# Optimization experiments

Measured on AMD Instinct MI355X. Metric: run time of the kernel, lower is better.

Reference implementation:

```python
import jax, jax.numpy as jnp
import numpy as np

N = 4096    # nodes per graph
C = 128     # in_channels == out_channels
HEAD = 1
E = 65536   # edges per graph (avg degree 16)


def setup_inputs() -> dict:
    key = jax.random.key(0)
    ks = jax.random.split(key, 24)
    def w(k, shape):
        return jax.random.normal(k, shape, dtype=jnp.float32) * 0.05
    return {
        "x1": jax.random.normal(ks[0], (N, C), dtype=jnp.float32),
        "x2": jax.random.normal(ks[1], (N, C), dtype=jnp.float32),
        "edge_index1": jax.random.randint(ks[2], (2, E), 0, N),
        "edge_index2": jax.random.randint(ks[3], (2, E), 0, N),
        "wl1_w": w(ks[4], (HEAD * C, C)), "wl1_b": w(ks[5], (HEAD * C,)),
        "wr1_w": w(ks[6], (HEAD * C, C)), "wr1_b": w(ks[7], (HEAD * C,)),
        "al1": w(ks[8], (HEAD, C)), "ar1": w(ks[9], (HEAD, C)),
        "wl2_w": w(ks[10], (HEAD * C, C)), "wl2_b": w(ks[11], (HEAD * C,)),
        "wr2_w": w(ks[12], (HEAD * C, C)), "wr2_b": w(ks[13], (HEAD * C,)),
        "al2": w(ks[14], (HEAD, C)), "ar2": w(ks[15], (HEAD, C)),
        "w1_w": w(ks[16], (C, 2 * C)), "w1_b": w(ks[17], (C,)),
        "w2_w": w(ks[18], (C, 2 * C)), "w2_b": w(ks[19], (C,)),
        "lin_w": w(ks[20], (HEAD * C, C)), "lin_b": w(ks[21], (HEAD * C,)),
    }


def _leaky_relu(x):
    return jnp.where(x > 0, x, 0.2 * x)


def _attention(src, tgt, wl, bl, wr, br, al, ar):
    # alpha_l: (N_src,), alpha_r: (N_tot,) -> dense (N_src, N_tot) softmax
    a_l = ((src @ wl.T + bl).reshape(-1, HEAD, C) * al[None]).sum(-1).mean(1)
    a_r = ((tgt @ wr.T + br).reshape(-1, HEAD, C) * ar[None]).sum(-1).mean(1)
    return jax.nn.softmax(_leaky_relu(a_l[:, None] + a_r[None, :]), axis=1)


def _aggr_update(x_i, tgt_all, ei, wl, bl, wr, br, al, ar, ww, wb):
    att = _attention(x_i, tgt_all, wl, bl, wr, br, al, ar)   # (N_i, N_tot)
    ot = x_i - att @ tgt_all                                  # (N_i, C)
    feat = jnp.concatenate([x_i, ot], axis=1)                 # (N_i, 2C)
    n = x_i.shape[0]
    loops = jnp.arange(n)                                     # add_self_loops
    src = jnp.concatenate([ei[0], loops])
    dst = jnp.concatenate([ei[1], loops])
    sums = jax.ops.segment_sum(feat[dst], src, num_segments=n)
    cnt = jax.ops.segment_sum(jnp.ones((src.shape[0],), feat.dtype), src, num_segments=n)
    aggr = sums / cnt[:, None]                                # scatter 'mean'
    return jax.nn.relu(aggr) @ ww.T + wb


def reference(x1, x2, edge_index1, edge_index2,
              wl1_w, wl1_b, wr1_w, wr1_b, al1, ar1,
              wl2_w, wl2_b, wr2_w, wr2_b, al2, ar2,
              w1_w, w1_b, w2_w, w2_b, lin_w, lin_b):
    Xs = [x1, x2]
    eis = [edge_index1, edge_index2]
    layers = [(wl1_w, wl1_b, wr1_w, wr1_b, al1, ar1, w1_w, w1_b),
              (wl2_w, wl2_b, wr2_w, wr2_b, al2, ar2, w2_w, w2_b)]
    for (wl, bl, wr, br, al, ar, ww, wb) in layers:
        tgt = jnp.concatenate(Xs, axis=0)
        Xs = [_aggr_update(Xs[i], tgt, eis[i], wl, bl, wr, br, al, ar, ww, wb)
              for i in range(2)]
    feats = jnp.concatenate(Xs, axis=0) @ lin_w.T + lin_b     # (2N, C)
    return jax.nn.sigmoid(feats @ feats.T)                    # (2N, 2N)
```

## Files before the change

### kernel.cpp

```cpp
#include <hip/hip_runtime.h>
#include <hip/hip_bf16.h>

#define NT 8192
#define NN 4096
#define CD 128
#define NE 65536

typedef __attribute__((ext_vector_type(8))) short bf16x8;
typedef __attribute__((ext_vector_type(16))) float f32x16;
typedef __attribute__((ext_vector_type(4))) float f32x4;

__global__ __launch_bounds__(256) void k_prep(
    const float* __restrict__ W1, const float* __restrict__ W2, const float* __restrict__ WL,
    float* __restrict__ WT1, float* __restrict__ WT2, float* __restrict__ WTL,
    const float* __restrict__ wlw0, const float* __restrict__ wlb0,
    const float* __restrict__ wrw0, const float* __restrict__ wrb0,
    const float* __restrict__ al0, const float* __restrict__ ar0,
    const float* __restrict__ wlw1, const float* __restrict__ wlb1,
    const float* __restrict__ wrw1, const float* __restrict__ wrb1,
    const float* __restrict__ al1, const float* __restrict__ ar1,
    float* __restrict__ VP, int* __restrict__ DEG) {
  int b = blockIdx.x, tid = threadIdx.x;
  if (b < 320) {
    int idx = b * 256 + tid;
    if (idx < 32768) { int c = idx >> 8, k = idx & 255; WT1[k * 128 + c] = W1[idx]; }
    else if (idx < 65536) { int j = idx - 32768; int c = j >> 8, k = j & 255; WT2[k * 128 + c] = W2[j]; }
    else { int j = idx - 65536; int c = j >> 7, k = j & 127; WTL[k * 128 + c] = WL[j]; }
  } else if (b < 322) {
    int L = b - 320;
    const float* wlw = L ? wlw1 : wlw0;
    const float* wlb = L ? wlb1 : wlb0;
    const float* wrw = L ? wrw1 : wrw0;
    const float* wrb = L ? wrb1 : wrb0;
    const float* alv = L ? al1 : al0;
    const float* arv = L ? ar1 : ar0;
    float* vp = VP + L * 258;
    if (tid < 128) {
      int c = tid;
      float sl = 0.f, sr = 0.f;
      for (int h = 0; h < 128; ++h) {
        sl += wlw[h * 128 + c] * alv[h];
        sr += wrw[h * 128 + c] * arv[h];
      }
      vp[c] = sl;
      vp[128 + c] = sr;
      if (c < 2) {
        const float* bb = c ? wrb : wlb;
        const float* aa = c ? arv : alv;
        float s = 0.f;
        for (int h = 0; h < 128; ++h) s += bb[h] * aa[h];
        vp[256 + c] = s;
      }
    }
  } else {
    int idx = (b - 322) * 256 + tid;
    DEG[idx] = 0;
  }
}

__global__ void k_deg(const int* __restrict__ EI1, const int* __restrict__ EI2,
                      int* __restrict__ DEG) {
  int idx = blockIdx.x * 256 + threadIdx.x;
  int g = idx >> 16, e = idx & 65535;
  const int* src = g ? EI2 : EI1;
  atomicAdd(&DEG[g * NN + src[e]], 1);
}

__global__ void k_scanoff(const int* __restrict__ DEG, int* __restrict__ OFFS,
                          int* __restrict__ CURS) {
  int g = blockIdx.x, tid = threadIdx.x;
  __shared__ int part[256];
  int loc[16];
  int s = 0;
  #pragma unroll
  for (int i = 0; i < 16; ++i) { loc[i] = s; s += DEG[g * NN + tid * 16 + i]; }
  part[tid] = s;
  __syncthreads();
  for (int d = 1; d < 256; d <<= 1) {
    int v = part[tid];
    int o = (tid >= d) ? part[tid - d] : 0;
    __syncthreads();
    part[tid] = v + o;
    __syncthreads();
  }
  int excl = tid ? part[tid - 1] : 0;
  #pragma unroll
  for (int i = 0; i < 16; ++i) {
    int o = excl + loc[i];
    OFFS[g * (NN + 1) + tid * 16 + i] = o;
    CURS[g * NN + tid * 16 + i] = o;
  }
  if (tid == 255) OFFS[g * (NN + 1) + NN] = part[255];
}

__global__ void k_fill(const int* __restrict__ EI1, const int* __restrict__ EI2,
                       int* __restrict__ CURS, int* __restrict__ ADJ) {
  int idx = blockIdx.x * 256 + threadIdx.x;
  int g = idx >> 16, e = idx & 65535;
  const int* ei = g ? EI2 : EI1;
  int s = ei[e], d = ei[NE + e];
  int pos = atomicAdd(&CURS[g * NN + s], 1);
  ADJ[g * NE + pos] = d;
}

__global__ void k_alar(const float* __restrict__ X, const float* __restrict__ VP,
                       float* __restrict__ AL, float* __restrict__ AR,
                       int* __restrict__ RANK) {
  if (blockIdx.x < 32) RANK[blockIdx.x * 256 + threadIdx.x] = 0;
  int lane = threadIdx.x & 63;
  int row = blockIdx.x * 4 + (threadIdx.x >> 6);
  float x0 = X[row * 128 + lane], x1 = X[row * 128 + 64 + lane];
  float sl = x0 * VP[lane] + x1 * VP[64 + lane];
  float sr = x0 * VP[128 + lane] + x1 * VP[192 + lane];
  #pragma unroll
  for (int m = 1; m < 64; m <<= 1) {
    sl += __shfl_xor(sl, m, 64);
    sr += __shfl_xor(sr, m, 64);
  }
  if (lane == 0) { AL[row] = sl + VP[256]; AR[row] = sr + VP[257]; }
}

__global__ void k_rank(const float* __restrict__ AR, int* __restrict__ RANK) {
  __shared__ float tile[1024];
  int j = blockIdx.x * 256 + threadIdx.x;
  int base = blockIdx.y * 1024;
  for (int t = threadIdx.x; t < 1024; t += 256) tile[t] = AR[base + t];
  __syncthreads();
  float aj = AR[j];
  int cnt = 0;
  #pragma unroll 8
  for (int u = 0; u < 1024; ++u) {
    float a2 = tile[u];
    cnt += (a2 < aj || (a2 == aj && (base + u) < j)) ? 1 : 0;
  }
  atomicAdd(&RANK[j], cnt);
}

__global__ void k_perm(const int* __restrict__ RANK, const float* __restrict__ AR,
                       int* __restrict__ PERM, float* __restrict__ ARS) {
  int j = blockIdx.x * 256 + threadIdx.x;
  int r = RANK[j];
  PERM[r] = j;
  ARS[r] = AR[j];
}

__global__ __launch_bounds__(320) void k_scanA(
    const float* __restrict__ X, const int* __restrict__ PERM,
    const float* __restrict__ ARS,
    float* __restrict__ P1, float* __restrict__ P2,
    float* __restrict__ CT1, float* __restrict__ CT2,
    float* __restrict__ Q1L, float* __restrict__ Q2L,
    float* __restrict__ QCT1, float* __restrict__ QCT2) {
  __shared__ int pc[64];
  __shared__ float w1[64], w2[64];
  int chunk = blockIdx.x, tid = threadIdx.x;
  if (tid < 64) {
    int r = chunk * 64 + tid;
    pc[tid] = PERM[r];
    float a = ARS[r];
    w1[tid] = __expf(a);
    w2[tid] = __expf(0.2f * a);
  }
  __syncthreads();
  if (tid < 128) {
    int c = tid;
    float acc = 0.f;
    #pragma unroll 4
    for (int t = 0; t < 64; ++t) {
      acc += w1[t] * X[pc[t] * 128 + c];
      P1[(chunk * 64 + t) * 128 + c] = acc;
    }
    CT1[chunk * 128 + c] = acc;
  } else if (tid < 256) {
    int c = tid - 128;
    float acc = 0.f;
    #pragma unroll 4
    for (int t = 0; t < 64; ++t) {
      acc += w2[t] * X[pc[t] * 128 + c];
      P2[(chunk * 64 + t) * 128 + c] = acc;
    }
    CT2[chunk * 128 + c] = acc;
  } else if (tid == 256) {
    float acc = 0.f;
    for (int t = 0; t < 64; ++t) { acc += w1[t]; Q1L[chunk * 64 + t] = acc; }
    QCT1[chunk] = acc;
  } else if (tid == 257) {
    float acc = 0.f;
    for (int t = 0; t < 64; ++t) { acc += w2[t]; Q2L[chunk * 64 + t] = acc; }
    QCT2[chunk] = acc;
  }
}

__global__ __launch_bounds__(320) void k_scanB(
    const float* __restrict__ CT1, const float* __restrict__ CT2,
    const float* __restrict__ QCT1, const float* __restrict__ QCT2,
    float* __restrict__ OFF1, float* __restrict__ OFF2,
    float* __restrict__ QOF1, float* __restrict__ QOF2) {
  int tid = threadIdx.x;
  if (tid < 128) {
    float acc = 0.f;
    #pragma unroll 8
    for (int ch = 0; ch < 128; ++ch) { acc += CT1[ch * 128 + tid]; OFF1[ch * 128 + tid] = acc; }
  } else if (tid < 256) {
    int c = tid - 128;
    float acc = 0.f;
    #pragma unroll 8
    for (int ch = 0; ch < 128; ++ch) { acc += CT2[ch * 128 + c]; OFF2[ch * 128 + c] = acc; }
  } else if (tid == 256) {
    float acc = 0.f;
    for (int ch = 0; ch < 128; ++ch) { acc += QCT1[ch]; QOF1[ch] = acc; }
  } else if (tid == 257) {
    float acc = 0.f;
    for (int ch = 0; ch < 128; ++ch) { acc += QCT2[ch]; QOF2[ch] = acc; }
  }
}

__global__ void k_combine(const float* __restrict__ X, const float* __restrict__ AL,
                          const float* __restrict__ ARS,
                          const float* __restrict__ P1, const float* __restrict__ P2,
                          const float* __restrict__ OFF1, const float* __restrict__ OFF2,
                          const float* __restrict__ Q1L, const float* __restrict__ Q2L,
                          const float* __restrict__ QOF1, const float* __restrict__ QOF2,
                          float* __restrict__ OT) {
  int row = blockIdx.x * 2 + (threadIdx.x >> 7);
  int c = threadIdx.x & 127;
  float ali = AL[row];
  float A1 = __expf(ali), A2 = __expf(0.2f * ali);
  float xv = -ali;
  int lo = 0, hi = NT;
  while (lo < hi) {
    int mid = (lo + hi) >> 1;
    if (ARS[mid] <= xv) lo = mid + 1; else hi = mid;
  }
  int b = lo - 1;
  float p1 = 0.f, p2 = 0.f, q1 = 0.f, q2 = 0.f;
  if (b >= 0) {
    int ch = b >> 6;
    p1 = P1[b * 128 + c] + (ch ? OFF1[(ch - 1) * 128 + c] : 0.f);
    p2 = P2[b * 128 + c] + (ch ? OFF2[(ch - 1) * 128 + c] : 0.f);
    q1 = Q1L[b] + (ch ? QOF1[ch - 1] : 0.f);
    q2 = Q2L[b] + (ch ? QOF2[ch - 1] : 0.f);
  }
  float T1 = OFF1[127 * 128 + c];
  float QT1 = QOF1[127];
  float num = A1 * (T1 - p1) + A2 * p2;
  float den = A1 * (QT1 - q1) + A2 * q2;
  OT[row * 128 + c] = X[row * 128 + c] - num / den;
}

__global__ __launch_bounds__(256) void k_aggr(const float* __restrict__ X,
                                              const float* __restrict__ OT,
                                              const int* __restrict__ OFFS,
                                              const int* __restrict__ ADJ,
                                              float* __restrict__ AGGR) {
  int node = blockIdx.x * 4 + (threadIdx.x >> 6);
  int lane = threadIdx.x & 63;
  int g = node >> 12, n = node & (NN - 1);
  const int* off = OFFS + g * (NN + 1);
  const int* adj = ADJ + g * NE;
  int beg = off[n], end = off[n + 1];
  const f32x4* src = (const f32x4*)((lane < 32 ? X : OT) + (size_t)g * NN * CD);
  int c4 = lane & 31;
  f32x4 acc = src[n * 32 + c4];
  for (int e = beg; e < end; ++e) {
    int d = adj[e];
    acc += src[d * 32 + c4];
  }
  f32x4 r = acc / (float)(end - beg + 1);
  ((f32x4*)AGGR)[(size_t)node * 64 + (lane < 32 ? c4 : 32 + c4)] = r;
}

template <int KD, bool RELU, bool OBF>
__global__ __launch_bounds__(128) void k_gemm(const float* __restrict__ A,
                                              const float* __restrict__ WT,
                                              const float* __restrict__ bias,
                                              void* __restrict__ out) {
  __shared__ float sA[8 * KD];
  int c = threadIdx.x;
  int r0 = blockIdx.x * 8;
  for (int i = c; i < 8 * KD; i += 128) {
    float a = A[(size_t)r0 * KD + i];
    if (RELU) a = fmaxf(a, 0.f);
    sA[i] = a;
  }
  __syncthreads();
  float acc[8];
  float bc = bias[c];
  #pragma unroll
  for (int i = 0; i < 8; ++i) acc[i] = bc;
  for (int k = 0; k < KD; ++k) {
    float wv = WT[k * 128 + c];
    #pragma unroll
    for (int i = 0; i < 8; ++i) acc[i] += sA[i * KD + k] * wv;
  }
  if (OBF) {
    __hip_bfloat16* o = (__hip_bfloat16*)out;
    #pragma unroll
    for (int i = 0; i < 8; ++i) o[(r0 + i) * 128 + c] = __float2bfloat16(acc[i]);
  } else {
    float* o = (float*)out;
    #pragma unroll
    for (int i = 0; i < 8; ++i) o[(r0 + i) * 128 + c] = acc[i];
  }
}

__device__ inline f32x16 zero16() {
  f32x16 v;
  #pragma unroll
  for (int i = 0; i < 16; ++i) v[i] = 0.f;
  return v;
}

__device__ inline void store_frag(float* __restrict__ out, const f32x16& a,
                                  int grow0, int gcol) {
  #pragma unroll
  for (int r = 0; r < 16; ++r) {
    int rloc = (r & 3) + 8 * (r >> 2);
    float v = a[r];
    out[(size_t)(grow0 + rloc) * 8192 + gcol] =
        __builtin_amdgcn_rcpf(1.f + __expf(-v));
  }
}

__global__ __launch_bounds__(256) void k_final(const unsigned short* __restrict__ F,
                                               float* __restrict__ out) {
  __shared__ unsigned short AT[128 * 128];
  __shared__ unsigned short BT[128 * 128];
  int cb = blockIdx.x, rb = blockIdx.y;
  int tid = threadIdx.x;
  #pragma unroll
  for (int q = 0; q < 8; ++q) {
    int idx = q * 256 + tid;
    int r = idx >> 4, ck = idx & 15;
    unsigned off = (unsigned)((r * 256 + ck * 16) ^ ((r & 7) << 4));
    uint4 va = *(const uint4*)(F + (size_t)(rb * 128 + r) * 128 + ck * 8);
    *(uint4*)((char*)AT + off) = va;
    uint4 vb = *(const uint4*)(F + (size_t)(cb * 128 + r) * 128 + ck * 8);
    *(uint4*)((char*)BT + off) = vb;
  }
  __syncthreads();
  int lane = tid & 63, w = tid >> 6;
  int wr = w >> 1, wc = w & 1;
  int l31 = lane & 31, kh = lane >> 5;
  int xorm = (l31 & 7) << 4;
  int rowA0 = wr * 64 + l31, rowA1 = rowA0 + 32;
  int rowB0 = wc * 64 + l31, rowB1 = rowB0 + 32;
  f32x16 a00 = zero16(), a01 = zero16(), a10 = zero16(), a11 = zero16();
  #pragma unroll
  for (int ks = 0; ks < 8; ++ks) {
    int kb = ks * 32 + kh * 16;
    bf16x8 av0 = *(const bf16x8*)((const char*)AT + ((rowA0 * 256 + kb) ^ xorm));
    bf16x8 av1 = *(const bf16x8*)((const char*)AT + ((rowA1 * 256 + kb) ^ xorm));
    bf16x8 bv0 = *(const bf16x8*)((const char*)BT + ((rowB0 * 256 + kb) ^ xorm));
    bf16x8 bv1 = *(const bf16x8*)((const char*)BT + ((rowB1 * 256 + kb) ^ xorm));
    a00 = __builtin_amdgcn_mfma_f32_32x32x16_bf16(av0, bv0, a00, 0, 0, 0);
    a01 = __builtin_amdgcn_mfma_f32_32x32x16_bf16(av0, bv1, a01, 0, 0, 0);
    a10 = __builtin_amdgcn_mfma_f32_32x32x16_bf16(av1, bv0, a10, 0, 0, 0);
    a11 = __builtin_amdgcn_mfma_f32_32x32x16_bf16(av1, bv1, a11, 0, 0, 0);
  }
  int grow = rb * 128 + wr * 64 + 4 * kh;
  int gcol = cb * 128 + wc * 64 + l31;
  store_frag(out, a00, grow, gcol);
  store_frag(out, a01, grow, gcol + 32);
  store_frag(out, a10, grow + 32, gcol);
  store_frag(out, a11, grow + 32, gcol + 32);
}

extern "C" void kernel_launch(void* const* d_in, const int* in_sizes, int n_in,
                              void* d_out, int out_size, void* d_ws, size_t ws_size,
                              hipStream_t stream) {
  (void)in_sizes; (void)n_in; (void)out_size; (void)ws_size;
  const float* x1 = (const float*)d_in[0];
  const float* x2 = (const float*)d_in[1];
  const int* ei1 = (const int*)d_in[2];
  const int* ei2 = (const int*)d_in[3];
  const float* wl_w[2] = {(const float*)d_in[4], (const float*)d_in[10]};
  const float* wl_b[2] = {(const float*)d_in[5], (const float*)d_in[11]};
  const float* wr_w[2] = {(const float*)d_in[6], (const float*)d_in[12]};
  const float* wr_b[2] = {(const float*)d_in[7], (const float*)d_in[13]};
  const float* alv[2] = {(const float*)d_in[8], (const float*)d_in[14]};
  const float* arv[2] = {(const float*)d_in[9], (const float*)d_in[15]};
  const float* ww_w[2] = {(const float*)d_in[16], (const float*)d_in[18]};
  const float* ww_b[2] = {(const float*)d_in[17], (const float*)d_in[19]};
  const float* lin_w = (const float*)d_in[20];
  const float* lin_b = (const float*)d_in[21];

  char* wp = (char*)d_ws;
  auto alloc = [&](size_t b) -> char* {
    char* p = wp;
    wp += (b + 255) & ~(size_t)255;
    return p;
  };
  float* XA = (float*)alloc((size_t)NT * CD * 4);
  float* XB = (float*)alloc((size_t)NT * CD * 4);
  float* OT = (float*)alloc((size_t)NT * CD * 4);
  float* P1 = (float*)alloc((size_t)NT * CD * 4);
  float* P2 = (float*)alloc((size_t)NT * CD * 4);
  float* AGGR = P1;
  float* CT1 = (float*)alloc(128 * 128 * 4);
  float* CT2 = (float*)alloc(128 * 128 * 4);
  float* OFF1 = (float*)alloc(128 * 128 * 4);
  float* OFF2 = (float*)alloc(128 * 128 * 4);
  float* AL = (float*)alloc(NT * 4);
  float* AR_ = (float*)alloc(NT * 4);
  float* ARS = (float*)alloc(NT * 4);
  float* Q1L = (float*)alloc(NT * 4);
  float* Q2L = (float*)alloc(NT * 4);
  float* QCT1 = (float*)alloc(128 * 4);
  float* QCT2 = (float*)alloc(128 * 4);
  float* QOF1 = (float*)alloc(128 * 4);
  float* QOF2 = (float*)alloc(128 * 4);
  float* VP = (float*)alloc(2 * 258 * 4);
  float* WT1 = (float*)alloc(256 * 128 * 4);
  float* WT2 = (float*)alloc(256 * 128 * 4);
  float* WTL = (float*)alloc(128 * 128 * 4);
  int* RANK = (int*)alloc(NT * 4);
  int* PERM = (int*)alloc(NT * 4);
  int* DEG = (int*)alloc(2 * NN * 4);
  int* OFFS = (int*)alloc(2 * (NN + 1) * 4);
  int* CURS = (int*)alloc(2 * NN * 4);
  int* ADJ = (int*)alloc(2 * NE * 4);
  unsigned short* FBF = (unsigned short*)OT;

  hipMemcpyAsync(XA, x1, (size_t)NN * CD * 4, hipMemcpyDeviceToDevice, stream);
  hipMemcpyAsync(XA + (size_t)NN * CD, x2, (size_t)NN * CD * 4, hipMemcpyDeviceToDevice, stream);
  k_prep<<<354, 256, 0, stream>>>(ww_w[0], ww_w[1], lin_w, WT1, WT2, WTL,
                                  wl_w[0], wl_b[0], wr_w[0], wr_b[0], alv[0], arv[0],
                                  wl_w[1], wl_b[1], wr_w[1], wr_b[1], alv[1], arv[1],
                                  VP, DEG);
  k_deg<<<512, 256, 0, stream>>>(ei1, ei2, DEG);
  k_scanoff<<<2, 256, 0, stream>>>(DEG, OFFS, CURS);
  k_fill<<<512, 256, 0, stream>>>(ei1, ei2, CURS, ADJ);

  float* X = XA;
  float* XN = XB;
  for (int L = 0; L < 2; ++L) {
    k_alar<<<2048, 256, 0, stream>>>(X, VP + L * 258, AL, AR_, RANK);
    k_rank<<<dim3(32, 8), 256, 0, stream>>>(AR_, RANK);
    k_perm<<<32, 256, 0, stream>>>(RANK, AR_, PERM, ARS);
    k_scanA<<<128, 320, 0, stream>>>(X, PERM, ARS, P1, P2, CT1, CT2, Q1L, Q2L, QCT1, QCT2);
    k_scanB<<<1, 320, 0, stream>>>(CT1, CT2, QCT1, QCT2, OFF1, OFF2, QOF1, QOF2);
    k_combine<<<4096, 256, 0, stream>>>(X, AL, ARS, P1, P2, OFF1, OFF2, Q1L, Q2L, QOF1, QOF2, OT);
    k_aggr<<<2048, 256, 0, stream>>>(X, OT, OFFS, ADJ, AGGR);
    k_gemm<256, true, false><<<1024, 128, 0, stream>>>(AGGR, L ? WT2 : WT1, ww_b[L], XN);
    float* t = X; X = XN; XN = t;
  }
  k_gemm<128, false, true><<<1024, 128, 0, stream>>>(X, WTL, lin_b, FBF);
  k_final<<<dim3(64, 64), 256, 0, stream>>>(FBF, (float*)d_out);
}
```

Baseline: 322.4 us.

## Fuse pipeline stages into fewer launches with last-block tail reductions

```diff
diff --git a/kernel.cpp b/kernel.cpp
--- a/kernel.cpp
+++ b/kernel.cpp
@@ -5,12 +5,24 @@
 #define NN 4096
 #define CD 128
 #define NE 65536
+#define SCOPE_AGT __HIP_MEMORY_SCOPE_AGENT
 
 typedef __attribute__((ext_vector_type(8))) short bf16x8;
 typedef __attribute__((ext_vector_type(16))) float f32x16;
 typedef __attribute__((ext_vector_type(4))) float f32x4;
 
+__device__ inline void stg_f(float* p, float v) {
+  __hip_atomic_store(p, v, __ATOMIC_RELAXED, SCOPE_AGT);
+}
+__device__ inline float ldg_f(const float* p) {
+  return __hip_atomic_load(p, __ATOMIC_RELAXED, SCOPE_AGT);
+}
+__device__ inline int ldg_i(const int* p) {
+  return __hip_atomic_load(p, __ATOMIC_RELAXED, SCOPE_AGT);
+}
+
 __global__ __launch_bounds__(256) void k_prep(
+    const float* __restrict__ x1, const float* __restrict__ x2, float* __restrict__ X,
     const float* __restrict__ W1, const float* __restrict__ W2, const float* __restrict__ WL,
     float* __restrict__ WT1, float* __restrict__ WT2, float* __restrict__ WTL,
     const float* __restrict__ wlw0, const float* __restrict__ wlb0,
@@ -19,15 +31,24 @@
     const float* __restrict__ wlw1, const float* __restrict__ wlb1,
     const float* __restrict__ wrw1, const float* __restrict__ wrb1,
     const float* __restrict__ al1, const float* __restrict__ ar1,
-    float* __restrict__ VP, int* __restrict__ DEG) {
+    float* __restrict__ VP, int* __restrict__ DEG, int* __restrict__ TK) {
   int b = blockIdx.x, tid = threadIdx.x;
-  if (b < 320) {
-    int idx = b * 256 + tid;
+  int gid = b * 256 + tid;
+  {
+    const f32x4* s1 = (const f32x4*)x1;
+    const f32x4* s2 = (const f32x4*)x2;
+    f32x4* d = (f32x4*)X;
+    d[gid] = s1[gid];
+    d[gid + NN * CD / 4] = s2[gid];
+  }
+  if (gid < 81920) {
+    int idx = gid;
     if (idx < 32768) { int c = idx >> 8, k = idx & 255; WT1[k * 128 + c] = W1[idx]; }
     else if (idx < 65536) { int j = idx - 32768; int c = j >> 8, k = j & 255; WT2[k * 128 + c] = W2[j]; }
     else { int j = idx - 65536; int c = j >> 7, k = j & 127; WTL[k * 128 + c] = WL[j]; }
-  } else if (b < 322) {
-    int L = b - 320;
+  }
+  if ((b == 508 || b == 509) && tid < 128) {
+    int L = b - 508;
     const float* wlw = L ? wlw1 : wlw0;
     const float* wlb = L ? wlb1 : wlb0;
     const float* wrw = L ? wrw1 : wrw0;
@@ -35,40 +56,159 @@
     const float* alv = L ? al1 : al0;
     const float* arv = L ? ar1 : ar0;
     float* vp = VP + L * 258;
-    if (tid < 128) {
-      int c = tid;
-      float sl = 0.f, sr = 0.f;
-      for (int h = 0; h < 128; ++h) {
-        sl += wlw[h * 128 + c] * alv[h];
-        sr += wrw[h * 128 + c] * arv[h];
-      }
-      vp[c] = sl;
-      vp[128 + c] = sr;
-      if (c < 2) {
-        const float* bb = c ? wrb : wlb;
-        const float* aa = c ? arv : alv;
-        float s = 0.f;
-        for (int h = 0; h < 128; ++h) s += bb[h] * aa[h];
-        vp[256 + c] = s;
-      }
-    }
+    int c = tid;
+    float sl = 0.f, sr = 0.f;
+    for (int h = 0; h < 128; ++h) {
+      sl += wlw[h * 128 + c] * alv[h];
+      sr += wrw[h * 128 + c] * arv[h];
+    }
+    vp[c] = sl;
+    vp[128 + c] = sr;
+    if (c < 2) {
+      const float* bb = c ? wrb : wlb;
+      const float* aa = c ? arv : alv;
+      float s = 0.f;
+      for (int h = 0; h < 128; ++h) s += bb[h] * aa[h];
+      vp[256 + c] = s;
+    }
+  }
+  if (gid < 2 * NN) DEG[gid] = 0;
+  if (b == 0 && tid < 8) TK[tid] = 0;
+}
+
+__device__ void alar_row(const float* __restrict__ X, const float* __restrict__ VP,
+                         float* __restrict__ AL, float* __restrict__ AR,
+                         int row, int lane) {
+  float x0 = X[row * 128 + lane], x1 = X[row * 128 + 64 + lane];
+  float sl = x0 * VP[lane] + x1 * VP[64 + lane];
+  float sr = x0 * VP[128 + lane] + x1 * VP[192 + lane];
+  #pragma unroll
+  for (int m = 1; m < 64; m <<= 1) {
+    sl += __shfl_xor(sl, m, 64);
+    sr += __shfl_xor(sr, m, 64);
+  }
+  if (lane == 0) { AL[row] = sl + VP[256]; AR[row] = sr + VP[257]; }
+}
+
+__device__ void rankperm_body(int rb, int tid, const float* __restrict__ AR,
+                              int* __restrict__ RANK, int* __restrict__ PERM,
+                              float* __restrict__ ARS, int* __restrict__ TK, int slot) {
+  __shared__ float tile[1024];
+  __shared__ int isLast;
+  int jb = rb & 31, tb = rb >> 5;
+  int base = tb * 1024;
+  for (int t = tid; t < 1024; t += 256) tile[t] = AR[base + t];
+  __syncthreads();
+  int j = jb * 256 + tid;
+  float aj = AR[j];
+  int cnt = 0;
+  #pragma unroll 8
+  for (int u = 0; u < 1024; ++u) {
+    float a2 = tile[u];
+    cnt += (a2 < aj || (a2 == aj && (base + u) < j)) ? 1 : 0;
+  }
+  atomicAdd(&RANK[j], cnt);
+  __threadfence();
+  __syncthreads();
+  if (tid == 0) {
+    int t = __hip_atomic_fetch_add(&TK[slot], 1, __ATOMIC_ACQ_REL, SCOPE_AGT);
+    isLast = (t == 255);
+  }
+  __syncthreads();
+  if (isLast) {
+    for (int jj = tid; jj < NT; jj += 256) {
+      int rk = ldg_i(&RANK[jj]);
+      PERM[rk] = jj;
+      ARS[rk] = AR[jj];
+    }
+  }
+}
+
+__device__ void scanA_body(int chunk, int tid, const float* __restrict__ X,
+                           const int* __restrict__ PERM, const float* __restrict__ ARS,
+                           float* __restrict__ P1, float* __restrict__ P2,
+                           float* __restrict__ CT1, float* __restrict__ CT2,
+                           float* __restrict__ Q1L, float* __restrict__ Q2L,
+                           float* __restrict__ QCT1, float* __restrict__ QCT2,
+                           float* __restrict__ OFF1, float* __restrict__ OFF2,
+                           float* __restrict__ QOF1, float* __restrict__ QOF2,
+                           int* __restrict__ TK, int slot) {
+  __shared__ float sm[192];
+  __shared__ int isLast;
+  int* pc = (int*)sm;
+  float* w1 = sm + 64;
+  float* w2 = sm + 128;
+  if (tid < 64) {
+    int r = chunk * 64 + tid;
+    pc[tid] = PERM[r];
+    float a = ARS[r];
+    w1[tid] = __expf(a);
+    w2[tid] = __expf(0.2f * a);
+  }
+  __syncthreads();
+  int c = tid & 127;
+  {
+    const float* W = (tid < 128) ? w1 : w2;
+    float* P = (tid < 128) ? P1 : P2;
+    float* CT = (tid < 128) ? CT1 : CT2;
+    float acc = 0.f;
+    #pragma unroll 4
+    for (int t = 0; t < 64; ++t) {
+      acc += W[t] * X[pc[t] * 128 + c];
+      P[(chunk * 64 + t) * 128 + c] = acc;
+    }
+    stg_f(&CT[chunk * 128 + c], acc);
+  }
+  if (tid < 2) {
+    const float* Wq = tid ? w2 : w1;
+    float* Q = tid ? Q2L : Q1L;
+    float* QC = tid ? QCT2 : QCT1;
+    float qa = 0.f;
+    for (int t = 0; t < 64; ++t) { qa += Wq[t]; Q[chunk * 64 + t] = qa; }
+    stg_f(&QC[chunk], qa);
+  }
+  __threadfence();
+  __syncthreads();
+  if (tid == 0) {
+    int t = __hip_atomic_fetch_add(&TK[slot], 1, __ATOMIC_ACQ_REL, SCOPE_AGT);
+    isLast = (t == 127);
+  }
+  __syncthreads();
+  if (isLast) {
+    const float* CTs = (tid < 128) ? CT1 : CT2;
+    float* OFF = (tid < 128) ? OFF1 : OFF2;
+    float a2 = 0.f;
+    #pragma unroll 8
+    for (int ch = 0; ch < 128; ++ch) { a2 += ldg_f(&CTs[ch * 128 + c]); OFF[ch * 128 + c] = a2; }
+    if (tid < 2) {
+      const float* QC = tid ? QCT2 : QCT1;
+      float* QO = tid ? QOF2 : QOF1;
+      float qa = 0.f;
+      for (int ch = 0; ch < 128; ++ch) { qa += ldg_f(&QC[ch]); QO[ch] = qa; }
+    }
+  }
+}
+
+__global__ __launch_bounds__(256) void k_stage2(
+    const int* __restrict__ EI1, const int* __restrict__ EI2, int* __restrict__ DEG,
+    const float* __restrict__ X, const float* __restrict__ VP0,
+    float* __restrict__ AL, float* __restrict__ AR, int* __restrict__ RANK) {
+  int b = blockIdx.x, tid = threadIdx.x;
+  if (b < 512) {
+    int gid = b * 256 + tid;
+    int g = gid >> 16, e = gid & 65535;
+    const int* src = g ? EI2 : EI1;
+    atomicAdd(&DEG[g * NN + src[e]], 1);
   } else {
-    int idx = (b - 322) * 256 + tid;
-    DEG[idx] = 0;
-  }
-}
-
-__global__ void k_deg(const int* __restrict__ EI1, const int* __restrict__ EI2,
-                      int* __restrict__ DEG) {
-  int idx = blockIdx.x * 256 + threadIdx.x;
-  int g = idx >> 16, e = idx & 65535;
-  const int* src = g ? EI2 : EI1;
-  atomicAdd(&DEG[g * NN + src[e]], 1);
-}
-
-__global__ void k_scanoff(const int* __restrict__ DEG, int* __restrict__ OFFS,
-                          int* __restrict__ CURS) {
-  int g = blockIdx.x, tid = threadIdx.x;
+    int bb = b - 512;
+    int gid = bb * 256 + tid;
+    if (gid < NT) RANK[gid] = 0;
+    alar_row(X, VP0, AL, AR, bb * 4 + (tid >> 6), tid & 63);
+  }
+}
+
+__device__ void scanoff_body(int g, int tid, const int* __restrict__ DEG,
+                             int* __restrict__ OFFS, int* __restrict__ CURS) {
   __shared__ int part[256];
   int loc[16];
   int s = 0;
@@ -93,126 +233,55 @@
   if (tid == 255) OFFS[g * (NN + 1) + NN] = part[255];
 }
 
-__global__ void k_fill(const int* __restrict__ EI1, const int* __restrict__ EI2,
-                       int* __restrict__ CURS, int* __restrict__ ADJ) {
-  int idx = blockIdx.x * 256 + threadIdx.x;
-  int g = idx >> 16, e = idx & 65535;
-  const int* ei = g ? EI2 : EI1;
-  int s = ei[e], d = ei[NE + e];
-  int pos = atomicAdd(&CURS[g * NN + s], 1);
-  ADJ[g * NE + pos] = d;
-}
-
-__global__ void k_alar(const float* __restrict__ X, const float* __restrict__ VP,
-                       float* __restrict__ AL, float* __restrict__ AR,
-                       int* __restrict__ RANK) {
-  if (blockIdx.x < 32) RANK[blockIdx.x * 256 + threadIdx.x] = 0;
-  int lane = threadIdx.x & 63;
-  int row = blockIdx.x * 4 + (threadIdx.x >> 6);
-  float x0 = X[row * 128 + lane], x1 = X[row * 128 + 64 + lane];
-  float sl = x0 * VP[lane] + x1 * VP[64 + lane];
-  float sr = x0 * VP[128 + lane] + x1 * VP[192 + lane];
-  #pragma unroll
-  for (int m = 1; m < 64; m <<= 1) {
-    sl += __shfl_xor(sl, m, 64);
-    sr += __shfl_xor(sr, m, 64);
-  }
-  if (lane == 0) { AL[row] = sl + VP[256]; AR[row] = sr + VP[257]; }
-}
-
-__global__ void k_rank(const float* __restrict__ AR, int* __restrict__ RANK) {
-  __shared__ float tile[1024];
-  int j = blockIdx.x * 256 + threadIdx.x;
-  int base = blockIdx.y * 1024;
-  for (int t = threadIdx.x; t < 1024; t += 256) tile[t] = AR[base + t];
-  __syncthreads();
-  float aj = AR[j];
-  int cnt = 0;
-  #pragma unroll 8
-  for (int u = 0; u < 1024; ++u) {
-    float a2 = tile[u];
-    cnt += (a2 < aj || (a2 == aj && (base + u) < j)) ? 1 : 0;
-  }
-  atomicAdd(&RANK[j], cnt);
-}
-
-__global__ void k_perm(const int* __restrict__ RANK, const float* __restrict__ AR,
-                       int* __restrict__ PERM, float* __restrict__ ARS) {
-  int j = blockIdx.x * 256 + threadIdx.x;
-  int r = RANK[j];
-  PERM[r] = j;
-  ARS[r] = AR[j];
-}
-
-__global__ __launch_bounds__(320) void k_scanA(
-    const float* __restrict__ X, const int* __restrict__ PERM,
-    const float* __restrict__ ARS,
+__global__ __launch_bounds__(256) void k_stage3(
+    const int* __restrict__ DEG, int* __restrict__ OFFS, int* __restrict__ CURS,
+    const float* __restrict__ AR, int* __restrict__ RANK, int* __restrict__ PERM,
+    float* __restrict__ ARS, int* __restrict__ TK) {
+  int b = blockIdx.x, tid = threadIdx.x;
+  if (b < 2) scanoff_body(b, tid, DEG, OFFS, CURS);
+  else rankperm_body(b - 2, tid, AR, RANK, PERM, ARS, TK, 0);
+}
+
+__global__ __launch_bounds__(256) void k_stage4(
+    const int* __restrict__ EI1, const int* __restrict__ EI2,
+    int* __restrict__ CURS, int* __restrict__ ADJ,
+    const float* __restrict__ X, const int* __restrict__ PERM, const float* __restrict__ ARS,
     float* __restrict__ P1, float* __restrict__ P2,
     float* __restrict__ CT1, float* __restrict__ CT2,
     float* __restrict__ Q1L, float* __restrict__ Q2L,
-    float* __restrict__ QCT1, float* __restrict__ QCT2) {
-  __shared__ int pc[64];
-  __shared__ float w1[64], w2[64];
-  int chunk = blockIdx.x, tid = threadIdx.x;
-  if (tid < 64) {
-    int r = chunk * 64 + tid;
-    pc[tid] = PERM[r];
-    float a = ARS[r];
-    w1[tid] = __expf(a);
-    w2[tid] = __expf(0.2f * a);
-  }
-  __syncthreads();
-  if (tid < 128) {
-    int c = tid;
-    float acc = 0.f;
-    #pragma unroll 4
-    for (int t = 0; t < 64; ++t) {
-      acc += w1[t] * X[pc[t] * 128 + c];
-      P1[(chunk * 64 + t) * 128 + c] = acc;
-    }
-    CT1[chunk * 128 + c] = acc;
-  } else if (tid < 256) {
-    int c = tid - 128;
-    float acc = 0.f;
-    #pragma unroll 4
-    for (int t = 0; t < 64; ++t) {
-      acc += w2[t] * X[pc[t] * 128 + c];
-      P2[(chunk * 64 + t) * 128 + c] = acc;
-    }
-    CT2[chunk * 128 + c] = acc;
-  } else if (tid == 256) {
-    float acc = 0.f;
-    for (int t = 0; t < 64; ++t) { acc += w1[t]; Q1L[chunk * 64 + t] = acc; }
-    QCT1[chunk] = acc;
-  } else if (tid == 257) {
-    float acc = 0.f;
-    for (int t = 0; t < 64; ++t) { acc += w2[t]; Q2L[chunk * 64 + t] = acc; }
-    QCT2[chunk] = acc;
-  }
-}
-
-__global__ __launch_bounds__(320) void k_scanB(
-    const float* __restrict__ CT1, const float* __restrict__ CT2,
-    const float* __restrict__ QCT1, const float* __restrict__ QCT2,
+    float* __restrict__ QCT1, float* __restrict__ QCT2,
     float* __restrict__ OFF1, float* __restrict__ OFF2,
-    float* __restrict__ QOF1, float* __restrict__ QOF2) {
-  int tid = threadIdx.x;
-  if (tid < 128) {
-    float acc = 0.f;
-    #pragma unroll 8
-    for (int ch = 0; ch < 128; ++ch) { acc += CT1[ch * 128 + tid]; OFF1[ch * 128 + tid] = acc; }
-  } else if (tid < 256) {
-    int c = tid - 128;
-    float acc = 0.f;
-    #pragma unroll 8
-    for (int ch = 0; ch < 128; ++ch) { acc += CT2[ch * 128 + c]; OFF2[ch * 128 + c] = acc; }
-  } else if (tid == 256) {
-    float acc = 0.f;
-    for (int ch = 0; ch < 128; ++ch) { acc += QCT1[ch]; QOF1[ch] = acc; }
-  } else if (tid == 257) {
-    float acc = 0.f;
-    for (int ch = 0; ch < 128; ++ch) { acc += QCT2[ch]; QOF2[ch] = acc; }
-  }
+    float* __restrict__ QOF1, float* __restrict__ QOF2, int* __restrict__ TK) {
+  int b = blockIdx.x, tid = threadIdx.x;
+  if (b < 512) {
+    int gid = b * 256 + tid;
+    int g = gid >> 16, e = gid & 65535;
+    const int* ei = g ? EI2 : EI1;
+    int s = ei[e], dn = ei[NE + e];
+    int pos = atomicAdd(&CURS[g * NN + s], 1);
+    ADJ[g * NE + pos] = dn;
+  } else {
+    scanA_body(b - 512, tid, X, PERM, ARS, P1, P2, CT1, CT2, Q1L, Q2L,
+               QCT1, QCT2, OFF1, OFF2, QOF1, QOF2, TK, 1);
+  }
+}
+
+__global__ __launch_bounds__(256) void k_rankperm1(
+    const float* __restrict__ AR, int* __restrict__ RANK, int* __restrict__ PERM,
+    float* __restrict__ ARS, int* __restrict__ TK) {
+  rankperm_body(blockIdx.x, threadIdx.x, AR, RANK, PERM, ARS, TK, 2);
+}
+
+__global__ __launch_bounds__(256) void k_scanA1(
+    const float* __restrict__ X, const int* __restrict__ PERM, const float* __restrict__ ARS,
+    float* __restrict__ P1, float* __restrict__ P2,
+    float* __restrict__ CT1, float* __restrict__ CT2,
+    float* __restrict__ Q1L, float* __restrict__ Q2L,
+    float* __restrict__ QCT1, float* __restrict__ QCT2,
+    float* __restrict__ OFF1, float* __restrict__ OFF2,
+    float* __restrict__ QOF1, float* __restrict__ QOF2, int* __restrict__ TK) {
+  scanA_body(blockIdx.x, threadIdx.x, X, PERM, ARS, P1, P2, CT1, CT2, Q1L, Q2L,
+             QCT1, QCT2, OFF1, OFF2, QOF1, QOF2, TK, 3);
 }
 
 __global__ void k_combine(const float* __restrict__ X, const float* __restrict__ AL,
@@ -232,14 +301,14 @@
     int mid = (lo + hi) >> 1;
     if (ARS[mid] <= xv) lo = mid + 1; else hi = mid;
   }
-  int b = lo - 1;
+  int bd = lo - 1;
   float p1 = 0.f, p2 = 0.f, q1 = 0.f, q2 = 0.f;
-  if (b >= 0) {
-    int ch = b >> 6;
-    p1 = P1[b * 128 + c] + (ch ? OFF1[(ch - 1) * 128 + c] : 0.f);
-    p2 = P2[b * 128 + c] + (ch ? OFF2[(ch - 1) * 128 + c] : 0.f);
-    q1 = Q1L[b] + (ch ? QOF1[ch - 1] : 0.f);
-    q2 = Q2L[b] + (ch ? QOF2[ch - 1] : 0.f);
+  if (bd >= 0) {
+    int ch = bd >> 6;
+    p1 = P1[bd * 128 + c] + (ch ? OFF1[(ch - 1) * 128 + c] : 0.f);
+    p2 = P2[bd * 128 + c] + (ch ? OFF2[(ch - 1) * 128 + c] : 0.f);
+    q1 = Q1L[bd] + (ch ? QOF1[ch - 1] : 0.f);
+    q2 = Q2L[bd] + (ch ? QOF2[ch - 1] : 0.f);
   }
   float T1 = OFF1[127 * 128 + c];
   float QT1 = QOF1[127];
@@ -248,59 +317,109 @@
   OT[row * 128 + c] = X[row * 128 + c] - num / den;
 }
 
-__global__ __launch_bounds__(256) void k_aggr(const float* __restrict__ X,
-                                              const float* __restrict__ OT,
-                                              const int* __restrict__ OFFS,
-                                              const int* __restrict__ ADJ,
-                                              float* __restrict__ AGGR) {
-  int node = blockIdx.x * 4 + (threadIdx.x >> 6);
-  int lane = threadIdx.x & 63;
-  int g = node >> 12, n = node & (NN - 1);
-  const int* off = OFFS + g * (NN + 1);
-  const int* adj = ADJ + g * NE;
-  int beg = off[n], end = off[n + 1];
-  const f32x4* src = (const f32x4*)((lane < 32 ? X : OT) + (size_t)g * NN * CD);
-  int c4 = lane & 31;
-  f32x4 acc = src[n * 32 + c4];
-  for (int e = beg; e < end; ++e) {
-    int d = adj[e];
-    acc += src[d * 32 + c4];
-  }
-  f32x4 r = acc / (float)(end - beg + 1);
-  ((f32x4*)AGGR)[(size_t)node * 64 + (lane < 32 ? c4 : 32 + c4)] = r;
-}
-
-template <int KD, bool RELU, bool OBF>
-__global__ __launch_bounds__(128) void k_gemm(const float* __restrict__ A,
-                                              const float* __restrict__ WT,
-                                              const float* __restrict__ bias,
-                                              void* __restrict__ out) {
-  __shared__ float sA[8 * KD];
-  int c = threadIdx.x;
-  int r0 = blockIdx.x * 8;
-  for (int i = c; i < 8 * KD; i += 128) {
-    float a = A[(size_t)r0 * KD + i];
-    if (RELU) a = fmaxf(a, 0.f);
-    sA[i] = a;
-  }
-  __syncthreads();
-  float acc[8];
-  float bc = bias[c];
-  #pragma unroll
-  for (int i = 0; i < 8; ++i) acc[i] = bc;
-  for (int k = 0; k < KD; ++k) {
-    float wv = WT[k * 128 + c];
+__global__ __launch_bounds__(256) void k_aggrgemm(
+    const float* __restrict__ X, const float* __restrict__ OT,
+    const int* __restrict__ OFFS, const int* __restrict__ ADJ,
+    const float* __restrict__ WT, const float* __restrict__ WB, float* __restrict__ XN,
+    int mode,
+    const float* __restrict__ VP1, float* __restrict__ AL, float* __restrict__ AR,
+    int* __restrict__ RANK,
+    const float* __restrict__ WTL, const float* __restrict__ LINB,
+    __hip_bfloat16* __restrict__ FBF) {
+  __shared__ float sA[8 * 256];
+  int b = blockIdx.x, tid = threadIdx.x;
+  int lane = tid & 63, wv = tid >> 6, c4 = lane & 31;
+  if (mode == 0) {
+    int gid = b * 256 + tid;
+    if (gid < NT) RANK[gid] = 0;
+  }
+  {
+    int beg[2], end[2];
+    const f32x4* srcp[2];
+    const int* adjp[2];
+    f32x4 acc[2];
     #pragma unroll
-    for (int i = 0; i < 8; ++i) acc[i] += sA[i * KD + k] * wv;
-  }
-  if (OBF) {
-    __hip_bfloat16* o = (__hip_bfloat16*)out;
+    for (int k = 0; k < 2; ++k) {
+      int node = b * 8 + wv * 2 + k;
+      int g = node >> 12, n = node & (NN - 1);
+      beg[k] = OFFS[g * (NN + 1) + n];
+      end[k] = OFFS[g * (NN + 1) + n + 1];
+      srcp[k] = (const f32x4*)((lane < 32 ? X : OT) + (size_t)g * NN * CD);
+      adjp[k] = ADJ + g * NE;
+      acc[k] = srcp[k][n * 32 + c4];
+    }
+    int maxd = max(end[0] - beg[0], end[1] - beg[1]);
+    for (int s = 0; s < maxd; ++s) {
+      #pragma unroll
+      for (int k = 0; k < 2; ++k) {
+        if (beg[k] + s < end[k]) acc[k] += srcp[k][adjp[k][beg[k] + s] * 32 + c4];
+      }
+    }
     #pragma unroll
-    for (int i = 0; i < 8; ++i) o[(r0 + i) * 128 + c] = __float2bfloat16(acc[i]);
+    for (int k = 0; k < 2; ++k) {
+      f32x4 r = acc[k] / (float)(end[k] - beg[k] + 1);
+      #pragma unroll
+      for (int q = 0; q < 4; ++q) r[q] = fmaxf(r[q], 0.f);
+      *(f32x4*)&sA[(wv * 2 + k) * 256 + (lane < 32 ? c4 * 4 : 128 + c4 * 4)] = r;
+    }
+  }
+  __syncthreads();
+  int c = tid & 127, half = tid >> 7;
+  float accv[4];
+  float bc = WB[c];
+  #pragma unroll
+  for (int i = 0; i < 4; ++i) accv[i] = bc;
+  for (int k4 = 0; k4 < 64; ++k4) {
+    float w0 = WT[(k4 * 4 + 0) * 128 + c];
+    float w1v = WT[(k4 * 4 + 1) * 128 + c];
+    float w2v = WT[(k4 * 4 + 2) * 128 + c];
+    float w3 = WT[(k4 * 4 + 3) * 128 + c];
+    #pragma unroll
+    for (int i = 0; i < 4; ++i) {
+      f32x4 av = *(const f32x4*)&sA[(half * 4 + i) * 256 + k4 * 4];
+      accv[i] += av[0] * w0 + av[1] * w1v + av[2] * w2v + av[3] * w3;
+    }
+  }
+  #pragma unroll
+  for (int i = 0; i < 4; ++i) XN[(size_t)(b * 8 + half * 4 + i) * 128 + c] = accv[i];
+  __syncthreads();
+  float* sB = sA;
+  #pragma unroll
+  for (int i = 0; i < 4; ++i) sB[(half * 4 + i) * 128 + c] = accv[i];
+  __syncthreads();
+  if (mode == 0) {
+    #pragma unroll
+    for (int k = 0; k < 2; ++k) {
+      int lr = wv * 2 + k;
+      float x0 = sB[lr * 128 + lane], x1 = sB[lr * 128 + 64 + lane];
+      float sl = x0 * VP1[lane] + x1 * VP1[64 + lane];
+      float sr = x0 * VP1[128 + lane] + x1 * VP1[192 + lane];
+      #pragma unroll
+      for (int m = 1; m < 64; m <<= 1) {
+        sl += __shfl_xor(sl, m, 64);
+        sr += __shfl_xor(sr, m, 64);
+      }
+      if (lane == 0) { AL[b * 8 + lr] = sl + VP1[256]; AR[b * 8 + lr] = sr + VP1[257]; }
+    }
   } else {
-    float* o = (float*)out;
+    float acl[4];
+    float lb = LINB[c];
     #pragma unroll
-    for (int i = 0; i < 8; ++i) o[(r0 + i) * 128 + c] = acc[i];
+    for (int i = 0; i < 4; ++i) acl[i] = lb;
+    for (int k4 = 0; k4 < 32; ++k4) {
+      float w0 = WTL[(k4 * 4 + 0) * 128 + c];
+      float w1v = WTL[(k4 * 4 + 1) * 128 + c];
+      float w2v = WTL[(k4 * 4 + 2) * 128 + c];
+      float w3 = WTL[(k4 * 4 + 3) * 128 + c];
+      #pragma unroll
+      for (int i = 0; i < 4; ++i) {
+        f32x4 av = *(const f32x4*)&sB[(half * 4 + i) * 128 + k4 * 4];
+        acl[i] += av[0] * w0 + av[1] * w1v + av[2] * w2v + av[3] * w3;
+      }
+    }
+    #pragma unroll
+    for (int i = 0; i < 4; ++i)
+      FBF[(size_t)(b * 8 + half * 4 + i) * 128 + c] = __float2bfloat16(acl[i]);
   }
 }
 
@@ -386,9 +505,9 @@
   const float* lin_b = (const float*)d_in[21];
 
   char* wp = (char*)d_ws;
-  auto alloc = [&](size_t b) -> char* {
+  auto alloc = [&](size_t bytes) -> char* {
     char* p = wp;
-    wp += (b + 255) & ~(size_t)255;
+    wp += (bytes + 255) & ~(size_t)255;
     return p;
   };
   float* XA = (float*)alloc((size_t)NT * CD * 4);
@@ -396,7 +515,7 @@
   float* OT = (float*)alloc((size_t)NT * CD * 4);
   float* P1 = (float*)alloc((size_t)NT * CD * 4);
   float* P2 = (float*)alloc((size_t)NT * CD * 4);
-  float* AGGR = P1;
+  __hip_bfloat16* FBF = (__hip_bfloat16*)alloc((size_t)NT * CD * 2);
   float* CT1 = (float*)alloc(128 * 128 * 4);
   float* CT2 = (float*)alloc(128 * 128 * 4);
   float* OFF1 = (float*)alloc(128 * 128 * 4);
@@ -420,31 +539,27 @@
   int* OFFS = (int*)alloc(2 * (NN + 1) * 4);
   int* CURS = (int*)alloc(2 * NN * 4);
   int* ADJ = (int*)alloc(2 * NE * 4);
-  unsigned short* FBF = (unsigned short*)OT;
-
-  hipMemcpyAsync(XA, x1, (size_t)NN * CD * 4, hipMemcpyDeviceToDevice, stream);
-  hipMemcpyAsync(XA + (size_t)NN * CD, x2, (size_t)NN * CD * 4, hipMemcpyDeviceToDevice, stream);
-  k_prep<<<354, 256, 0, stream>>>(ww_w[0], ww_w[1], lin_w, WT1, WT2, WTL,
+  int* TK = (int*)alloc(8 * 4);
+
+  k_prep<<<512, 256, 0, stream>>>(x1, x2, XA, ww_w[0], ww_w[1], lin_w, WT1, WT2, WTL,
                                   wl_w[0], wl_b[0], wr_w[0], wr_b[0], alv[0], arv[0],
                                   wl_w[1], wl_b[1], wr_w[1], wr_b[1], alv[1], arv[1],
-                                  VP, DEG);
-  k_deg<<<512, 256, 0, stream>>>(ei1, ei2, DEG);
-  k_scanoff<<<2, 256, 0, stream>>>(DEG, OFFS, CURS);
-  k_fill<<<512, 256, 0, stream>>>(ei1, ei2, CURS, ADJ);
-
-  float* X = XA;
-  float* XN = XB;
-  for (int L = 0; L < 2; ++L) {
-    k_alar<<<2048, 256, 0, stream>>>(X, VP + L * 258, AL, AR_, RANK);
-    k_rank<<<dim3(32, 8), 256, 0, stream>>>(AR_, RANK);
-    k_perm<<<32, 256, 0, stream>>>(RANK, AR_, PERM, ARS);
-    k_scanA<<<128, 320, 0, stream>>>(X, PERM, ARS, P1, P2, CT1, CT2, Q1L, Q2L, QCT1, QCT2);
-    k_scanB<<<1, 320, 0, stream>>>(CT1, CT2, QCT1, QCT2, OFF1, OFF2, QOF1, QOF2);
-    k_combine<<<4096, 256, 0, stream>>>(X, AL, ARS, P1, P2, OFF1, OFF2, Q1L, Q2L, QOF1, QOF2, OT);
-    k_aggr<<<2048, 256, 0, stream>>>(X, OT, OFFS, ADJ, AGGR);
-    k_gemm<256, true, false><<<1024, 128, 0, stream>>>(AGGR, L ? WT2 : WT1, ww_b[L], XN);
-    float* t = X; X = XN; XN = t;
-  }
-  k_gemm<128, false, true><<<1024, 128, 0, stream>>>(X, WTL, lin_b, FBF);
-  k_final<<<dim3(64, 64), 256, 0, stream>>>(FBF, (float*)d_out);
-}
+                                  VP, DEG, TK);
+  k_stage2<<<2560, 256, 0, stream>>>(ei1, ei2, DEG, XA, VP, AL, AR_, RANK);
+  k_stage3<<<258, 256, 0, stream>>>(DEG, OFFS, CURS, AR_, RANK, PERM, ARS, TK);
+  k_stage4<<<640, 256, 0, stream>>>(ei1, ei2, CURS, ADJ, XA, PERM, ARS,
+                                    P1, P2, CT1, CT2, Q1L, Q2L, QCT1, QCT2,
+                                    OFF1, OFF2, QOF1, QOF2, TK);
+  k_combine<<<4096, 256, 0, stream>>>(XA, AL, ARS, P1, P2, OFF1, OFF2, Q1L, Q2L,
+                                      QOF1, QOF2, OT);
+  k_aggrgemm<<<1024, 256, 0, stream>>>(XA, OT, OFFS, ADJ, WT1, ww_b[0], XB,
+                                       0, VP + 258, AL, AR_, RANK, WTL, lin_b, FBF);
+  k_rankperm1<<<256, 256, 0, stream>>>(AR_, RANK, PERM, ARS, TK);
+  k_scanA1<<<128, 256, 0, stream>>>(XB, PERM, ARS, P1, P2, CT1, CT2, Q1L, Q2L,
+                                    QCT1, QCT2, OFF1, OFF2, QOF1, QOF2, TK);
+  k_combine<<<4096, 256, 0, stream>>>(XB, AL, ARS, P1, P2, OFF1, OFF2, Q1L, Q2L,
+                                      QOF1, QOF2, OT);
+  k_aggrgemm<<<1024, 256, 0, stream>>>(XB, OT, OFFS, ADJ, WT2, ww_b[1], XA,
+                                       1, VP, AL, AR_, RANK, WTL, lin_b, FBF);
+  k_final<<<dim3(64, 64), 256, 0, stream>>>((const unsigned short*)FBF, (float*)d_out);
+}
```

Result: slower. 450.7 us (+39.8%).
